# Performance work log

Measured on AMD Instinct MI355X. Metric: run time of the kernel, lower is better.

The kernel has to match this reference:

```python
import jax, jax.numpy as jnp
import numpy as np

B, S, I, H, C, V = 512, 64, 300, 1024, 2, 50000


def setup_inputs() -> dict:
    key = jax.random.key(0)
    ks = jax.random.split(key, 10)
    s = 0.05
    return {
        "x": jax.random.randint(ks[0], (B, S), 0, V),
        "lengths": jax.random.randint(ks[1], (B,), 1, S + 1),
        "embed": jax.random.normal(ks[2], (V, I), jnp.float32) * s,
        "Wih_e": jax.random.normal(ks[3], (4 * H, I), jnp.float32) * s,
        "Whh_e": jax.random.normal(ks[4], (4 * H, H), jnp.float32) * s,
        "bih_e": jnp.zeros((4 * H,), jnp.float32),
        "bhh_e": jnp.zeros((4 * H,), jnp.float32),
        "Wih_d": jax.random.normal(ks[5], (4 * H, I), jnp.float32) * s,
        "Whh_d": jax.random.normal(ks[6], (4 * H, H), jnp.float32) * s,
        "bih_d": jnp.zeros((4 * H,), jnp.float32),
        "bhh_d": jnp.zeros((4 * H,), jnp.float32),
        "W_lin": jax.random.normal(ks[7], (C, H), jnp.float32) * s,
        "b_lin": jnp.zeros((C,), jnp.float32),
    }


def lstm_cell(xi, h, c, Wih, Whh, bih, bhh):
    # PyTorch LSTMCell gate order: i, f, g, o
    g = xi @ Wih.T + bih + h @ Whh.T + bhh
    i, f, gg, o = jnp.split(g, 4, axis=-1)
    c = jax.nn.sigmoid(f) * c + jax.nn.sigmoid(i) * jnp.tanh(gg)
    return jax.nn.sigmoid(o) * jnp.tanh(c), c


def reference(x, lengths, embed, Wih_e, Whh_e, bih_e, bhh_e,
              Wih_d, Whh_d, bih_d, bhh_d, W_lin, b_lin):
    bsz, slen = x.shape
    hdim = Whh_e.shape[1]
    ncls = W_lin.shape[0]
    xs = embed[x.T]                      # [S, B, I] (seq-major, like x.transpose(0,1))

    h0 = jnp.zeros((bsz, hdim), xs.dtype)
    c0 = jnp.zeros((bsz, hdim), xs.dtype)

    def enc_step(carry, xi):
        h, c = carry
        h, c = lstm_cell(xi, h, c, Wih_e, Whh_e, bih_e, bhh_e)
        return (h, c), h

    # forward pass over sequence
    (h, c), enc_fwd = jax.lax.scan(enc_step, (h0, c0), xs)          # enc_fwd: [S,B,H]
    # backward pass with the SAME encoder cell, continuing from (h, c)
    (h, c), h_bwd = jax.lax.scan(enc_step, (h, c), xs[::-1])        # h_bwd:  [S,B,H]
    # k-th backward step pairs with encoder_forward[k] in the original code
    enc_out = (enc_fwd + h_bwd) * 0.5                               # [S,B,H]

    def dec_step(carry, xi):
        h, c = carry
        # original attention sums over batch AND hidden -> one scalar per timestep,
        # and rebuilds w as a fresh Variable (no gradient through the weights).
        w = jax.nn.softmax(jnp.sum(h[None, :, :] * enc_out, axis=(1, 2)))  # [S]
        w = jax.lax.stop_gradient(w)
        h = h + jnp.einsum('t,tbh->bh', w, enc_out)
        h, c = lstm_cell(xi, h, c, Wih_d, Whh_d, bih_d, bhh_d)
        return (h, c), h

    _, dec = jax.lax.scan(dec_step, (h, c), xs)                     # [S,B,H]

    out = dec @ W_lin.T + b_lin                                     # [S,B,C]
    out = out.transpose(1, 0, 2)                                    # [B,S,C]
    pad = jnp.array([1.0, 0.0], out.dtype)                          # overwrite beyond lengths
    mask = jnp.arange(slen)[None, :] < lengths[:, None]             # [B,S]
    out = jnp.where(mask[:, :, None], out, pad)
    return out.reshape(bsz * slen, ncls)
```

## Files before the change

kernel.cpp:

```cpp
#include <hip/hip_runtime.h>
#include <hip/hip_bf16.h>

#define BSZ 512
#define SEQ 64
#define IDIM 300
#define KP1 384
#define HDIM 1024
#define G4 4096
#define BH (BSZ*HDIM)

typedef __attribute__((ext_vector_type(8))) short bf16x8;
typedef __attribute__((ext_vector_type(4))) float f32x4;
typedef __attribute__((ext_vector_type(8))) unsigned short u16x8;
typedef __attribute__((ext_vector_type(4))) unsigned short u16x4;

__device__ __forceinline__ float sigmoidf_(float x){ return 1.f/(1.f+__expf(-x)); }
__device__ __forceinline__ float bf2f(unsigned short u){
    union{unsigned int i; float f;} v; v.i = ((unsigned)u)<<16; return v.f;
}
__device__ __forceinline__ unsigned short f2bf(float f){
    __hip_bfloat16 b = __float2bfloat16(f);
    return *(unsigned short*)&b;
}

__global__ void embed_gather_k(const int* __restrict__ x, const float* __restrict__ embed,
                               __hip_bfloat16* __restrict__ xs){
    int t = blockIdx.x, b = blockIdx.y;
    int ix = x[b*SEQ + t];
    const float* src = embed + (size_t)ix * IDIM;
    __hip_bfloat16* dst = xs + ((size_t)t*BSZ + b) * KP1;
    for (int k = threadIdx.x; k < KP1; k += 64)
        dst[k] = __float2bfloat16(k < IDIM ? src[k] : 0.f);
}

__global__ void conv_w_k(const float* __restrict__ Wih_e, const float* __restrict__ Wih_d,
                         const float* __restrict__ Whh_e, const float* __restrict__ Whh_d,
                         __hip_bfloat16* __restrict__ Pe, __hip_bfloat16* __restrict__ Pd,
                         __hip_bfloat16* __restrict__ He, __hip_bfloat16* __restrict__ Hd){
    int nr = blockIdx.x, v = blockIdx.y;
    int orig = ((nr>>5)&3)*HDIM + (nr>>7)*32 + (nr&31);
    if (v < 2){
        const float* src = (v ? Wih_d : Wih_e) + (size_t)orig*IDIM;
        __hip_bfloat16* dst = (v ? Pd : Pe) + (size_t)nr*KP1;
        for (int k = threadIdx.x; k < KP1; k += 64)
            dst[k] = __float2bfloat16(k < IDIM ? src[k] : 0.f);
    } else {
        const float* src = ((v == 3) ? Whh_d : Whh_e) + (size_t)orig*HDIM;
        __hip_bfloat16* dst = ((v == 3) ? Hd : He) + (size_t)nr*HDIM;
        for (int k = threadIdx.x; k < HDIM; k += 64)
            dst[k] = __float2bfloat16(src[k]);
    }
}

__global__ void bias_comb_k(const float* __restrict__ a, const float* __restrict__ b2,
                            const float* __restrict__ c2, const float* __restrict__ d2,
                            float* __restrict__ be, float* __restrict__ bd){
    int i = blockIdx.x*256 + threadIdx.x;
    int nr = i & 4095;
    int orig = ((nr>>5)&3)*HDIM + (nr>>7)*32 + (nr&31);
    if (i < G4) be[nr] = a[orig] + b2[orig];
    else        bd[nr] = c2[orig] + d2[orig];
}

__global__ void zero_hc_k(float* __restrict__ h, float* __restrict__ c,
                          __hip_bfloat16* __restrict__ h_bf,
                          unsigned int* __restrict__ bar, unsigned int* __restrict__ gen){
    int idx = blockIdx.x*256 + threadIdx.x;
    h[idx] = 0.f; c[idx] = 0.f; h_bf[idx] = __float2bfloat16(0.f);
    if (idx == 0){ bar[0] = 0u; gen[0] = 0u; }
}

#define BM 64
#define BN 128
#define NK1 (KP1/128)
#define NK2 (HDIM/128)
#define NKT (NK1+NK2)

__global__ __launch_bounds__(512) void xpre_k(
    const __hip_bfloat16* __restrict__ xs, const __hip_bfloat16* __restrict__ B1,
    float* __restrict__ Gx)
{
    __shared__ __align__(16) char smem[131072];
    const int tid  = threadIdx.x;
    const int lane = tid & 63, wv = tid >> 6;
    const int row0 = blockIdx.y * BM;
    const int col0 = blockIdx.x * BN;
    const int wm = wv >> 2, wn = wv & 3;
    const int fb = blockIdx.y*32 + blockIdx.x;

    #pragma unroll
    for (int ks = 0; ks < 3; ++ks)
        #pragma unroll
        for (int q = 0; q < 4; ++q){
            int u = q*512 + tid;
            int r = u >> 4, s = u & 15;
            int g = s ^ (r & 15);
            const __hip_bfloat16* src = B1 + (size_t)(col0 + r)*KP1 + ks*128 + g*8;
            char* dst = smem + ks*32768 + q*8192 + wv*1024;
            __builtin_amdgcn_global_load_lds(
                (const __attribute__((address_space(1))) void*)src,
                (__attribute__((address_space(3))) void*)dst, 16, 0, 0);
        }

    auto stage_a = [&](int t, int ks, int p){
        #pragma unroll
        for (int half = 0; half < 2; ++half){
            int u = half*512 + tid;
            int r = u >> 4, s = u & 15;
            int g = s ^ (r & 15);
            const __hip_bfloat16* src = xs + (size_t)t*BSZ*KP1 + (size_t)(row0 + r)*KP1 + ks*128 + g*8;
            char* dst = smem + 98304 + p*16384 + half*8192 + wv*1024;
            __builtin_amdgcn_global_load_lds(
                (const __attribute__((address_space(1))) void*)src,
                (__attribute__((address_space(3))) void*)dst, 16, 0, 0);
        }
    };

    f32x4 acc[2][2] = {};
    auto compute_a = [&](int p, int ks){
        const char* Ab = smem + 98304 + p*16384;
        const char* Bb = smem + ks*32768;
        const int rr = lane & 15, g = lane >> 4;
        bf16x8 af[2][4], bfr[2][4];
        #pragma unroll
        for (int m = 0; m < 2; ++m){
            int r = wm*32 + m*16 + rr;
            #pragma unroll
            for (int kk = 0; kk < 4; ++kk)
                af[m][kk] = *(const bf16x8*)(Ab + r*256 + ((kk*4 + g) ^ (r & 15))*16);
        }
        #pragma unroll
        for (int n = 0; n < 2; ++n){
            int r = wn*32 + n*16 + rr;
            #pragma unroll
            for (int kk = 0; kk < 4; ++kk)
                bfr[n][kk] = *(const bf16x8*)(Bb + r*256 + ((kk*4 + g) ^ (r & 15))*16);
        }
        #pragma unroll
        for (int kk = 0; kk < 4; ++kk)
            #pragma unroll
            for (int m = 0; m < 2; ++m)
                #pragma unroll
                for (int n = 0; n < 2; ++n)
                    acc[m][n] = __builtin_amdgcn_mfma_f32_16x16x32_bf16(af[m][kk], bfr[n][kk], acc[m][n], 0, 0, 0);
    };

    stage_a(0, 0, 0);
    __syncthreads();
    for (int t = 0; t < SEQ; ++t){
        #pragma unroll
        for (int ks = 0; ks < 3; ++ks){
            int u = t*3 + ks;
            int p = u & 1;
            if (u + 1 < SEQ*3) stage_a((u+1)/3, (u+1)%3, p ^ 1);
            compute_a(p, ks);
            if (ks == 2){
                float* gp = Gx + (((size_t)t*256 + fb)*512 + tid)*16;
                #pragma unroll
                for (int m = 0; m < 2; ++m)
                    #pragma unroll
                    for (int n = 0; n < 2; ++n)
                        *(f32x4*)(gp + (m*2+n)*4) = acc[m][n];
                acc[0][0] = f32x4{}; acc[0][1] = f32x4{};
                acc[1][0] = f32x4{}; acc[1][1] = f32x4{};
            }
            __syncthreads();
        }
    }
}

__device__ __forceinline__ void grid_sync_(unsigned int* bar, unsigned int* gen){
    __syncthreads();
    __threadfence();
    if (threadIdx.x == 0){
        unsigned int g = __hip_atomic_load(gen, __ATOMIC_RELAXED, __HIP_MEMORY_SCOPE_AGENT);
        if (__hip_atomic_fetch_add(bar, 1u, __ATOMIC_ACQ_REL, __HIP_MEMORY_SCOPE_AGENT) == 255u){
            __hip_atomic_store(bar, 0u, __ATOMIC_RELAXED, __HIP_MEMORY_SCOPE_AGENT);
            __hip_atomic_fetch_add(gen, 1u, __ATOMIC_RELEASE, __HIP_MEMORY_SCOPE_AGENT);
        } else {
            while (__hip_atomic_load(gen, __ATOMIC_ACQUIRE, __HIP_MEMORY_SCOPE_AGENT) == g)
                __builtin_amdgcn_s_sleep(2);
        }
    }
    __syncthreads();
    __threadfence();
}

__global__ __launch_bounds__(512, 2) void enc_persist_k(
    const __hip_bfloat16* __restrict__ B2, const float* __restrict__ bias,
    const float* __restrict__ Gx,
    float* __restrict__ c, float* __restrict__ h, __hip_bfloat16* __restrict__ h_bf,
    __hip_bfloat16* __restrict__ enc,
    unsigned int* __restrict__ bar, unsigned int* __restrict__ gen)
{
    __shared__ __align__(16) char smem[98304];
    const int tid  = threadIdx.x;
    const int lane = tid & 63, wv = tid >> 6;
    const int bid  = blockIdx.x;
    const int bx = bid & 31, by = bid >> 5;
    const int row0 = by * BM;
    const int col0 = bx * BN;
    const int wm = wv >> 2, wn = wv & 3;

    const int erow = tid >> 3;
    const int ejj0 = (tid & 7) * 4;
    const size_t ebase = (size_t)(row0 + erow)*HDIM + bx*32 + ejj0;

    f32x4 creg = {0.f, 0.f, 0.f, 0.f};

    auto stage = [&](int ks, int p){
        char* base = smem + p*49152;
        #pragma unroll
        for (int half = 0; half < 2; ++half){
            int u = half*512 + tid;
            int r = u >> 4, s = u & 15;
            int g = s ^ (r & 15);
            const __hip_bfloat16* src = h_bf + (size_t)(row0 + r)*HDIM + ks*128 + g*8;
            char* dst = base + half*8192 + wv*1024;
            __builtin_amdgcn_global_load_lds(
                (const __attribute__((address_space(1))) void*)src,
                (__attribute__((address_space(3))) void*)dst, 16, 0, 0);
        }
        #pragma unroll
        for (int q = 0; q < 4; ++q){
            int u = q*512 + tid;
            int r = u >> 4, s = u & 15;
            int g = s ^ (r & 15);
            const __hip_bfloat16* src = B2 + (size_t)(col0 + r)*HDIM + ks*128 + g*8;
            char* dst = base + 16384 + q*8192 + wv*1024;
            __builtin_amdgcn_global_load_lds(
                (const __attribute__((address_space(1))) void*)src,
                (__attribute__((address_space(3))) void*)dst, 16, 0, 0);
        }
    };

    for (int i = 0; i < 2*SEQ; ++i){
        const int t = (i < SEQ) ? i : (2*SEQ - 1 - i);
        f32x4 acc[2][2];
        {
            const float* gp = Gx + (((size_t)t*256 + bid)*512 + tid)*16;
            #pragma unroll
            for (int m = 0; m < 2; ++m)
                #pragma unroll
                for (int n = 0; n < 2; ++n)
                    acc[m][n] = *(const f32x4*)(gp + (m*2+n)*4);
        }

        stage(0, 0);
        __syncthreads();
        for (int ks = 0; ks < NK2; ++ks){
            int p = ks & 1;
            if (ks + 1 < NK2) stage(ks + 1, p ^ 1);
            {
                const char* Ab = smem + p*49152;
                const char* Bb = Ab + 16384;
                const int rr = lane & 15, g = lane >> 4;
                bf16x8 af[2][4], bfr[2][4];
                #pragma unroll
                for (int m = 0; m < 2; ++m){
                    int r = wm*32 + m*16 + rr;
                    #pragma unroll
                    for (int kk = 0; kk < 4; ++kk)
                        af[m][kk] = *(const bf16x8*)(Ab + r*256 + ((kk*4 + g) ^ (r & 15))*16);
                }
                #pragma unroll
                for (int n = 0; n < 2; ++n){
                    int r = wn*32 + n*16 + rr;
                    #pragma unroll
                    for (int kk = 0; kk < 4; ++kk)
                        bfr[n][kk] = *(const bf16x8*)(Bb + r*256 + ((kk*4 + g) ^ (r & 15))*16);
                }
                #pragma unroll
                for (int kk = 0; kk < 4; ++kk)
                    #pragma unroll
                    for (int m = 0; m < 2; ++m)
                        #pragma unroll
                        for (int n = 0; n < 2; ++n)
                            acc[m][n] = __builtin_amdgcn_mfma_f32_16x16x32_bf16(af[m][kk], bfr[n][kk], acc[m][n], 0, 0, 0);
            }
            __syncthreads();
        }

        float* ep = (float*)smem;
        {
            const int rr = lane & 15, q4 = lane >> 4;
            #pragma unroll
            for (int m = 0; m < 2; ++m){
                int row = wm*32 + m*16 + q4*4;
                #pragma unroll
                for (int n = 0; n < 2; ++n){
                    int jj = n*16 + rr;
                    float bi = bias[col0 + wn*32 + jj];
                    #pragma unroll
                    for (int q = 0; q < 4; ++q)
                        ep[(wn*64 + row + q)*33 + jj] = acc[m][n][q] + bi;
                }
            }
        }
        __syncthreads();
        {
            f32x4 hv;
            #pragma unroll
            for (int e = 0; e < 4; ++e){
                float gi = ep[(0*64 + erow)*33 + ejj0 + e];
                float gf = ep[(1*64 + erow)*33 + ejj0 + e];
                float gg = ep[(2*64 + erow)*33 + ejj0 + e];
                float go = ep[(3*64 + erow)*33 + ejj0 + e];
                float cc = sigmoidf_(gf)*creg[e] + sigmoidf_(gi)*tanhf(gg);
                float hh = sigmoidf_(go)*tanhf(cc);
                creg[e] = cc; hv[e] = hh;
            }
            u16x4 hb;
            #pragma unroll
            for (int e = 0; e < 4; ++e) hb[e] = f2bf(hv[e]);
            *(u16x4*)(h_bf + ebase) = hb;
            if (i < SEQ){
                *(u16x4*)(enc + (size_t)i*BH + ebase) = hb;
            } else {
                __hip_bfloat16* eslot = enc + (size_t)(i - SEQ)*BH;
                u16x4 eo = *(const u16x4*)(eslot + ebase);
                u16x4 r;
                #pragma unroll
                for (int e = 0; e < 4; ++e) r[e] = f2bf(0.5f*(bf2f(eo[e]) + hv[e]));
                *(u16x4*)(eslot + ebase) = r;
            }
            if (i == 2*SEQ - 1){
                *(f32x4*)(c + ebase) = creg;
                *(f32x4*)(h + ebase) = hv;
            }
        }
        grid_sync_(bar, gen);
    }
}

template<int XPRE>
__global__ __launch_bounds__(512) void lstm_step_k(
    const __hip_bfloat16* __restrict__ A1, const __hip_bfloat16* __restrict__ B1,
    const __hip_bfloat16* __restrict__ A2, const __hip_bfloat16* __restrict__ B2,
    const float* __restrict__ bias, const float* __restrict__ Gxt,
    float* __restrict__ c, float* __restrict__ h, __hip_bfloat16* __restrict__ h_bf,
    __hip_bfloat16* __restrict__ encSlot, int mode)
{
    constexpr int NKT_ = XPRE ? NK2 : NKT;
    __shared__ __align__(16) char smem[98304];
    const int tid  = threadIdx.x;
    const int lane = tid & 63, wv = tid >> 6;
    const int row0 = blockIdx.y * BM;
    const int col0 = blockIdx.x * BN;
    const int wm = wv >> 2, wn = wv & 3;

    f32x4 acc[2][2];
    if constexpr (XPRE){
        const float* gp = Gxt + (((size_t)(blockIdx.y*32 + blockIdx.x))*512 + tid)*16;
        #pragma unroll
        for (int m = 0; m < 2; ++m)
            #pragma unroll
            for (int n = 0; n < 2; ++n)
                acc[m][n] = *(const f32x4*)(gp + (m*2+n)*4);
    } else {
        acc[0][0] = f32x4{}; acc[0][1] = f32x4{};
        acc[1][0] = f32x4{}; acc[1][1] = f32x4{};
    }

    auto stage = [&](int ks, int p){
        const __hip_bfloat16* A; const __hip_bfloat16* B; int KA, k0;
        if constexpr (XPRE){ A = A2; B = B2; KA = HDIM; k0 = ks*128; }
        else {
            if (ks < NK1){ A = A1; B = B1; KA = KP1;  k0 = ks*128; }
            else         { A = A2; B = B2; KA = HDIM; k0 = (ks-NK1)*128; }
        }
        char* base = smem + p*49152;
        #pragma unroll
        for (int half = 0; half < 2; ++half){
            int u = half*512 + tid;
            int r = u >> 4, s = u & 15;
            int g = s ^ (r & 15);
            const __hip_bfloat16* src = A + (size_t)(row0 + r)*KA + k0 + g*8;
            char* dst = base + half*8192 + wv*1024;
            __builtin_amdgcn_global_load_lds(
                (const __attribute__((address_space(1))) void*)src,
                (__attribute__((address_space(3))) void*)dst, 16, 0, 0);
        }
        #pragma unroll
        for (int q = 0; q < 4; ++q){
            int u = q*512 + tid;
            int r = u >> 4, s = u & 15;
            int g = s ^ (r & 15);
            const __hip_bfloat16* src = B + (size_t)(col0 + r)*KA + k0 + g*8;
            char* dst = base + 16384 + q*8192 + wv*1024;
            __builtin_amdgcn_global_load_lds(
                (const __attribute__((address_space(1))) void*)src,
                (__attribute__((address_space(3))) void*)dst, 16, 0, 0);
        }
    };

    auto compute = [&](int p){
        const char* Ab = smem + p*49152;
        const char* Bb = Ab + 16384;
        const int rr = lane & 15, g = lane >> 4;
        bf16x8 af[2][4], bfr[2][4];
        #pragma unroll
        for (int m = 0; m < 2; ++m){
            int r = wm*32 + m*16 + rr;
            #pragma unroll
            for (int kk = 0; kk < 4; ++kk)
                af[m][kk] = *(const bf16x8*)(Ab + r*256 + ((kk*4 + g) ^ (r & 15))*16);
        }
        #pragma unroll
        for (int n = 0; n < 2; ++n){
            int r = wn*32 + n*16 + rr;
            #pragma unroll
            for (int kk = 0; kk < 4; ++kk)
                bfr[n][kk] = *(const bf16x8*)(Bb + r*256 + ((kk*4 + g) ^ (r & 15))*16);
        }
        #pragma unroll
        for (int kk = 0; kk < 4; ++kk)
            #pragma unroll
            for (int m = 0; m < 2; ++m)
                #pragma unroll
                for (int n = 0; n < 2; ++n)
                    acc[m][n] = __builtin_amdgcn_mfma_f32_16x16x32_bf16(af[m][kk], bfr[n][kk], acc[m][n], 0, 0, 0);
    };

    const int erow = tid >> 3;
    const int ejj0 = (tid & 7) * 4;
    const size_t ebase = (size_t)(row0 + erow)*HDIM + blockIdx.x*32 + ejj0;

    stage(0, 0);
    const f32x4 cpre = *(const f32x4*)(c + ebase);
    __syncthreads();
    for (int ks = 0; ks < NKT_; ++ks){
        int p = ks & 1;
        if (ks + 1 < NKT_) stage(ks + 1, p ^ 1);
        compute(p);
        __syncthreads();
    }

    float* ep = (float*)smem;
    {
        const int rr = lane & 15, q4 = lane >> 4;
        #pragma unroll
        for (int m = 0; m < 2; ++m){
            int row = wm*32 + m*16 + q4*4;
            #pragma unroll
            for (int n = 0; n < 2; ++n){
                int jj = n*16 + rr;
                float bi = bias[col0 + wn*32 + jj];
                #pragma unroll
                for (int q = 0; q < 4; ++q)
                    ep[(wn*64 + row + q)*33 + jj] = acc[m][n][q] + bi;
            }
        }
    }
    __syncthreads();
    {
        f32x4 cv, hv;
        #pragma unroll
        for (int e = 0; e < 4; ++e){
            float gi = ep[(0*64 + erow)*33 + ejj0 + e];
            float gf = ep[(1*64 + erow)*33 + ejj0 + e];
            float gg = ep[(2*64 + erow)*33 + ejj0 + e];
            float go = ep[(3*64 + erow)*33 + ejj0 + e];
            float cc = sigmoidf_(gf)*cpre[e] + sigmoidf_(gi)*tanhf(gg);
            float hh = sigmoidf_(go)*tanhf(cc);
            cv[e] = cc; hv[e] = hh;
        }
        *(f32x4*)(c + ebase) = cv;
        *(f32x4*)(h + ebase) = hv;
        u16x4 hb;
        #pragma unroll
        for (int e = 0; e < 4; ++e) hb[e] = f2bf(hv[e]);
        *(u16x4*)(h_bf + ebase) = hb;
        if (mode == 0){
            *(u16x4*)(encSlot + ebase) = hb;
        } else if (mode == 1){
            u16x4 eo = *(const u16x4*)(encSlot + ebase);
            u16x4 r;
            #pragma unroll
            for (int e = 0; e < 4; ++e) r[e] = f2bf(0.5f*(bf2f(eo[e]) + hv[e]));
            *(u16x4*)(encSlot + ebase) = r;
        }
    }
}

__global__ __launch_bounds__(256) void attn_part_k(
    const __hip_bfloat16* __restrict__ h_bf, const __hip_bfloat16* __restrict__ enc,
    float* __restrict__ part,
    const float* __restrict__ h, const float* __restrict__ Wl, const float* __restrict__ bl,
    const int* __restrict__ len, float* __restrict__ out, int dect)
{
    __shared__ float red[4];
    int lane = threadIdx.x & 63, w = threadIdx.x >> 6;
    if (blockIdx.x < 64){
        int ch = blockIdx.x;
        int s  = blockIdx.y;
        const u16x8* e  = (const u16x8*)(enc + (size_t)s*BH + (size_t)ch*8192);
        const u16x8* hp = (const u16x8*)(h_bf + (size_t)ch*8192);
        float sum = 0.f;
        for (int i = threadIdx.x; i < 1024; i += 256){
            u16x8 ev = e[i], hv = hp[i];
            #pragma unroll
            for (int j = 0; j < 8; ++j) sum += bf2f(hv[j]) * bf2f(ev[j]);
        }
        #pragma unroll
        for (int m = 32; m >= 1; m >>= 1) sum += __shfl_xor(sum, m);
        if (lane == 0) red[w] = sum;
        __syncthreads();
        if (threadIdx.x == 0) part[s*64 + ch] = red[0]+red[1]+red[2]+red[3];
    } else if (dect >= 0){
        int b = ((blockIdx.x - 64)*64 + blockIdx.y)*4 + w;
        const float* hb = h + (size_t)b*HDIM;
        float s0 = 0.f, s1 = 0.f;
        for (int j = lane; j < HDIM; j += 64){
            float v = hb[j];
            s0 += v * Wl[j];
            s1 += v * Wl[HDIM + j];
        }
        #pragma unroll
        for (int m = 32; m >= 1; m >>= 1){ s0 += __shfl_xor(s0, m); s1 += __shfl_xor(s1, m); }
        if (lane == 0){
            bool valid = dect < len[b];
            size_t r = ((size_t)b*SEQ + dect)*2;
            out[r]   = valid ? (s0 + bl[0]) : 1.0f;
            out[r+1] = valid ? (s1 + bl[1]) : 0.0f;
        }
    }
}

__global__ __launch_bounds__(256) void attn_apply_k(
    const float* __restrict__ h, const float* __restrict__ part,
    const __hip_bfloat16* __restrict__ enc, __hip_bfloat16* __restrict__ hat_bf)
{
    __shared__ float wl[64];
    int lane = threadIdx.x & 63;
    if (threadIdx.x < 64){
        float tot = 0.f;
        #pragma unroll 8
        for (int ch = 0; ch < 64; ++ch) tot += part[lane*64 + ch];
        float m = tot;
        #pragma unroll
        for (int msk = 32; msk >= 1; msk >>= 1) m = fmaxf(m, __shfl_xor(m, msk));
        float e = __expf(tot - m);
        float sm = e;
        #pragma unroll
        for (int msk = 32; msk >= 1; msk >>= 1) sm += __shfl_xor(sm, msk);
        wl[lane] = e / sm;
    }
    __syncthreads();
    size_t i4 = ((size_t)blockIdx.x*256 + threadIdx.x) * 4;
    float v[4];
    {
        f32x4 a = *(const f32x4*)(h + i4);
        v[0]=a[0]; v[1]=a[1]; v[2]=a[2]; v[3]=a[3];
    }
    for (int s = 0; s < SEQ; ++s){
        u16x4 ev = *(const u16x4*)(enc + (size_t)s*BH + i4);
        float w = wl[s];
        #pragma unroll
        for (int j = 0; j < 4; ++j) v[j] += w * bf2f(ev[j]);
    }
    u16x4 ov;
    #pragma unroll
    for (int j = 0; j < 4; ++j) ov[j] = f2bf(v[j]);
    *(u16x4*)(hat_bf + i4) = ov;
}

__global__ void dec_linear_k(const float* __restrict__ h, const float* __restrict__ Wl,
                             const float* __restrict__ bl, const int* __restrict__ len,
                             float* __restrict__ out, int t)
{
    int b = blockIdx.x, lane = threadIdx.x;
    const float* hb = h + (size_t)b*HDIM;
    float s0 = 0.f, s1 = 0.f;
    for (int j = lane; j < HDIM; j += 64){
        float v = hb[j];
        s0 += v * Wl[j];
        s1 += v * Wl[HDIM + j];
    }
    #pragma unroll
    for (int m = 32; m >= 1; m >>= 1){ s0 += __shfl_xor(s0, m); s1 += __shfl_xor(s1, m); }
    if (lane == 0){
        bool valid = t < len[b];
        size_t r = ((size_t)b*SEQ + t)*2;
        out[r]   = valid ? (s0 + bl[0]) : 1.0f;
        out[r+1] = valid ? (s1 + bl[1]) : 0.0f;
    }
}

extern "C" void kernel_launch(void* const* d_in, const int* in_sizes, int n_in,
                              void* d_out, int out_size, void* d_ws, size_t ws_size,
                              hipStream_t stream)
{
    (void)in_sizes; (void)n_in; (void)out_size;
    const int*   x      = (const int*)  d_in[0];
    const int*   len    = (const int*)  d_in[1];
    const float* embed  = (const float*)d_in[2];
    const float* Wih_e  = (const float*)d_in[3];
    const float* Whh_e  = (const float*)d_in[4];
    const float* bih_e  = (const float*)d_in[5];
    const float* bhh_e  = (const float*)d_in[6];
    const float* Wih_d  = (const float*)d_in[7];
    const float* Whh_d  = (const float*)d_in[8];
    const float* bih_d  = (const float*)d_in[9];
    const float* bhh_d  = (const float*)d_in[10];
    const float* W_lin  = (const float*)d_in[11];
    const float* b_lin  = (const float*)d_in[12];
    float* out = (float*)d_out;

    float* ws = (float*)d_ws;
    size_t off = 0;
    auto alloc = [&](size_t nfloats){ size_t o = off; off += (nfloats + 63) & ~(size_t)63; return o; };
    __hip_bfloat16* xs_bf  = (__hip_bfloat16*)(ws + alloc((size_t)SEQ*BSZ*KP1/2));
    __hip_bfloat16* Pe     = (__hip_bfloat16*)(ws + alloc((size_t)G4*KP1/2));
    __hip_bfloat16* Pd     = (__hip_bfloat16*)(ws + alloc((size_t)G4*KP1/2));
    __hip_bfloat16* He     = (__hip_bfloat16*)(ws + alloc((size_t)G4*HDIM/2));
    __hip_bfloat16* Hd     = (__hip_bfloat16*)(ws + alloc((size_t)G4*HDIM/2));
    float* be   = ws + alloc(G4);
    float* bd   = ws + alloc(G4);
    float* h    = ws + alloc(BH);
    float* c    = ws + alloc(BH);
    __hip_bfloat16* h_bf   = (__hip_bfloat16*)(ws + alloc(BH/2));
    __hip_bfloat16* hat_bf = (__hip_bfloat16*)(ws + alloc(BH/2));
    __hip_bfloat16* enc    = (__hip_bfloat16*)(ws + alloc((size_t)SEQ*BH/2));
    float* part = ws + alloc(64*64);
    unsigned int* bar = (unsigned int*)(ws + alloc(32));
    unsigned int* gen = bar + 16;
    float* Gx   = ws + alloc((size_t)SEQ*256*512*16);
    const bool useGx = (off * sizeof(float)) <= ws_size;

    embed_gather_k<<<dim3(SEQ, BSZ), 64, 0, stream>>>(x, embed, xs_bf);
    conv_w_k<<<dim3(G4, 4), 64, 0, stream>>>(Wih_e, Wih_d, Whh_e, Whh_d, Pe, Pd, He, Hd);
    bias_comb_k<<<32, 256, 0, stream>>>(bih_e, bhh_e, bih_d, bhh_d, be, bd);
    zero_hc_k<<<BH/256, 256, 0, stream>>>(h, c, h_bf, bar, gen);

    dim3 ggrid(G4/BN, BSZ/BM);

    if (useGx){
        xpre_k<<<dim3(32, 8), 512, 0, stream>>>(xs_bf, Pe, Gx);
        enc_persist_k<<<256, 512, 0, stream>>>(He, be, Gx, c, h, h_bf, enc, bar, gen);
    } else {
        for (int t = 0; t < SEQ; ++t)
            lstm_step_k<0><<<ggrid, 512, 0, stream>>>(xs_bf + (size_t)t*BSZ*KP1, Pe, h_bf, He, be,
                                                      nullptr, c, h, h_bf, enc + (size_t)t*BH, 0);
        for (int k = 0; k < SEQ; ++k){
            int t = SEQ - 1 - k;
            lstm_step_k<0><<<ggrid, 512, 0, stream>>>(xs_bf + (size_t)t*BSZ*KP1, Pe, h_bf, He, be,
                                                      nullptr, c, h, h_bf, enc + (size_t)k*BH, 1);
        }
    }

    for (int t = 0; t < SEQ; ++t){
        attn_part_k<<<dim3(66, 64), 256, 0, stream>>>(h_bf, enc, part, h, W_lin, b_lin, len, out, t - 1);
        attn_apply_k<<<512, 256, 0, stream>>>(h, part, enc, hat_bf);
        lstm_step_k<0><<<ggrid, 512, 0, stream>>>(xs_bf + (size_t)t*BSZ*KP1, Pd, hat_bf, Hd, bd,
                                                  nullptr, c, h, h_bf, nullptr, 2);
    }
    dec_linear_k<<<BSZ, 64, 0, stream>>>(h, W_lin, b_lin, len, out, SEQ - 1);
}
```

Baseline: 4.341 ms.

## Fold input projection into persistent encoder kernel and drop precomputed Gx buffer

Removes the separate xpre_k kernel that precomputed the input-to-gate GEMM for all timesteps into a large fp32 Gx buffer. The persistent encoder now streams both the embedded input tiles and the recurrent h tiles through the same double-buffered K loop every step. It also drops the trailing threadfence in the grid barrier and the 2-blocks-per-CU launch bound. This saves the large Gx write/read traffic and one kernel launch, but puts the input GEMM back on the serial recurrent critical path.

Measured after the change: 11.24 ms. +159.0%, slower.

```diff
diff --git a/kernel.cpp b/kernel.cpp
--- a/kernel.cpp
+++ b/kernel.cpp
@@ -76,99 +76,6 @@
 #define NK2 (HDIM/128)
 #define NKT (NK1+NK2)
 
-__global__ __launch_bounds__(512) void xpre_k(
-    const __hip_bfloat16* __restrict__ xs, const __hip_bfloat16* __restrict__ B1,
-    float* __restrict__ Gx)
-{
-    __shared__ __align__(16) char smem[131072];
-    const int tid  = threadIdx.x;
-    const int lane = tid & 63, wv = tid >> 6;
-    const int row0 = blockIdx.y * BM;
-    const int col0 = blockIdx.x * BN;
-    const int wm = wv >> 2, wn = wv & 3;
-    const int fb = blockIdx.y*32 + blockIdx.x;
-
-    #pragma unroll
-    for (int ks = 0; ks < 3; ++ks)
-        #pragma unroll
-        for (int q = 0; q < 4; ++q){
-            int u = q*512 + tid;
-            int r = u >> 4, s = u & 15;
-            int g = s ^ (r & 15);
-            const __hip_bfloat16* src = B1 + (size_t)(col0 + r)*KP1 + ks*128 + g*8;
-            char* dst = smem + ks*32768 + q*8192 + wv*1024;
-            __builtin_amdgcn_global_load_lds(
-                (const __attribute__((address_space(1))) void*)src,
-                (__attribute__((address_space(3))) void*)dst, 16, 0, 0);
-        }
-
-    auto stage_a = [&](int t, int ks, int p){
-        #pragma unroll
-        for (int half = 0; half < 2; ++half){
-            int u = half*512 + tid;
-            int r = u >> 4, s = u & 15;
-            int g = s ^ (r & 15);
-            const __hip_bfloat16* src = xs + (size_t)t*BSZ*KP1 + (size_t)(row0 + r)*KP1 + ks*128 + g*8;
-            char* dst = smem + 98304 + p*16384 + half*8192 + wv*1024;
-            __builtin_amdgcn_global_load_lds(
-                (const __attribute__((address_space(1))) void*)src,
-                (__attribute__((address_space(3))) void*)dst, 16, 0, 0);
-        }
-    };
-
-    f32x4 acc[2][2] = {};
-    auto compute_a = [&](int p, int ks){
-        const char* Ab = smem + 98304 + p*16384;
-        const char* Bb = smem + ks*32768;
-        const int rr = lane & 15, g = lane >> 4;
-        bf16x8 af[2][4], bfr[2][4];
-        #pragma unroll
-        for (int m = 0; m < 2; ++m){
-            int r = wm*32 + m*16 + rr;
-            #pragma unroll
-            for (int kk = 0; kk < 4; ++kk)
-                af[m][kk] = *(const bf16x8*)(Ab + r*256 + ((kk*4 + g) ^ (r & 15))*16);
-        }
-        #pragma unroll
-        for (int n = 0; n < 2; ++n){
-            int r = wn*32 + n*16 + rr;
-            #pragma unroll
-            for (int kk = 0; kk < 4; ++kk)
-                bfr[n][kk] = *(const bf16x8*)(Bb + r*256 + ((kk*4 + g) ^ (r & 15))*16);
-        }
-        #pragma unroll
-        for (int kk = 0; kk < 4; ++kk)
-            #pragma unroll
-            for (int m = 0; m < 2; ++m)
-                #pragma unroll
-                for (int n = 0; n < 2; ++n)
-                    acc[m][n] = __builtin_amdgcn_mfma_f32_16x16x32_bf16(af[m][kk], bfr[n][kk], acc[m][n], 0, 0, 0);
-    };
-
-    stage_a(0, 0, 0);
-    __syncthreads();
-    for (int t = 0; t < SEQ; ++t){
-        #pragma unroll
-        for (int ks = 0; ks < 3; ++ks){
-            int u = t*3 + ks;
-            int p = u & 1;
-            if (u + 1 < SEQ*3) stage_a((u+1)/3, (u+1)%3, p ^ 1);
-            compute_a(p, ks);
-            if (ks == 2){
-                float* gp = Gx + (((size_t)t*256 + fb)*512 + tid)*16;
-                #pragma unroll
-                for (int m = 0; m < 2; ++m)
-                    #pragma unroll
-                    for (int n = 0; n < 2; ++n)
-                        *(f32x4*)(gp + (m*2+n)*4) = acc[m][n];
-                acc[0][0] = f32x4{}; acc[0][1] = f32x4{};
-                acc[1][0] = f32x4{}; acc[1][1] = f32x4{};
-            }
-            __syncthreads();
-        }
-    }
-}
-
 __device__ __forceinline__ void grid_sync_(unsigned int* bar, unsigned int* gen){
     __syncthreads();
     __threadfence();
@@ -183,12 +90,11 @@
         }
     }
     __syncthreads();
-    __threadfence();
-}
-
-__global__ __launch_bounds__(512, 2) void enc_persist_k(
+}
+
+__global__ __launch_bounds__(512) void enc_persist_k(
+    const __hip_bfloat16* __restrict__ xs, const __hip_bfloat16* __restrict__ B1,
     const __hip_bfloat16* __restrict__ B2, const float* __restrict__ bias,
-    const float* __restrict__ Gx,
     float* __restrict__ c, float* __restrict__ h, __hip_bfloat16* __restrict__ h_bf,
     __hip_bfloat16* __restrict__ enc,
     unsigned int* __restrict__ bar, unsigned int* __restrict__ gen)
@@ -208,49 +114,46 @@
 
     f32x4 creg = {0.f, 0.f, 0.f, 0.f};
 
-    auto stage = [&](int ks, int p){
-        char* base = smem + p*49152;
-        #pragma unroll
-        for (int half = 0; half < 2; ++half){
-            int u = half*512 + tid;
-            int r = u >> 4, s = u & 15;
-            int g = s ^ (r & 15);
-            const __hip_bfloat16* src = h_bf + (size_t)(row0 + r)*HDIM + ks*128 + g*8;
-            char* dst = base + half*8192 + wv*1024;
-            __builtin_amdgcn_global_load_lds(
-                (const __attribute__((address_space(1))) void*)src,
-                (__attribute__((address_space(3))) void*)dst, 16, 0, 0);
-        }
-        #pragma unroll
-        for (int q = 0; q < 4; ++q){
-            int u = q*512 + tid;
-            int r = u >> 4, s = u & 15;
-            int g = s ^ (r & 15);
-            const __hip_bfloat16* src = B2 + (size_t)(col0 + r)*HDIM + ks*128 + g*8;
-            char* dst = base + 16384 + q*8192 + wv*1024;
-            __builtin_amdgcn_global_load_lds(
-                (const __attribute__((address_space(1))) void*)src,
-                (__attribute__((address_space(3))) void*)dst, 16, 0, 0);
-        }
-    };
-
     for (int i = 0; i < 2*SEQ; ++i){
         const int t = (i < SEQ) ? i : (2*SEQ - 1 - i);
-        f32x4 acc[2][2];
-        {
-            const float* gp = Gx + (((size_t)t*256 + bid)*512 + tid)*16;
-            #pragma unroll
-            for (int m = 0; m < 2; ++m)
-                #pragma unroll
-                for (int n = 0; n < 2; ++n)
-                    acc[m][n] = *(const f32x4*)(gp + (m*2+n)*4);
-        }
+        const __hip_bfloat16* A1 = xs + (size_t)t*BSZ*KP1;
+
+        auto stage = [&](int ks, int p){
+            const __hip_bfloat16* A; const __hip_bfloat16* B; int KA, k0;
+            if (ks < NK1){ A = A1;   B = B1; KA = KP1;  k0 = ks*128; }
+            else         { A = h_bf; B = B2; KA = HDIM; k0 = (ks-NK1)*128; }
+            char* base = smem + p*49152;
+            #pragma unroll
+            for (int half = 0; half < 2; ++half){
+                int u = half*512 + tid;
+                int r = u >> 4, s = u & 15;
+                int g = s ^ (r & 15);
+                const __hip_bfloat16* src = A + (size_t)(row0 + r)*KA + k0 + g*8;
+                char* dst = base + half*8192 + wv*1024;
+                __builtin_amdgcn_global_load_lds(
+                    (const __attribute__((address_space(1))) void*)src,
+                    (__attribute__((address_space(3))) void*)dst, 16, 0, 0);
+            }
+            #pragma unroll
+            for (int q = 0; q < 4; ++q){
+                int u = q*512 + tid;
+                int r = u >> 4, s = u & 15;
+                int g = s ^ (r & 15);
+                const __hip_bfloat16* src = B + (size_t)(col0 + r)*KA + k0 + g*8;
+                char* dst = base + 16384 + q*8192 + wv*1024;
+                __builtin_amdgcn_global_load_lds(
+                    (const __attribute__((address_space(1))) void*)src,
+                    (__attribute__((address_space(3))) void*)dst, 16, 0, 0);
+            }
+        };
+
+        f32x4 acc[2][2] = {};
 
         stage(0, 0);
         __syncthreads();
-        for (int ks = 0; ks < NK2; ++ks){
+        for (int ks = 0; ks < NKT; ++ks){
             int p = ks & 1;
-            if (ks + 1 < NK2) stage(ks + 1, p ^ 1);
+            if (ks + 1 < NKT) stage(ks + 1, p ^ 1);
             {
                 const char* Ab = smem + p*49152;
                 const char* Bb = Ab + 16384;
@@ -333,15 +236,13 @@
     }
 }
 
-template<int XPRE>
 __global__ __launch_bounds__(512) void lstm_step_k(
     const __hip_bfloat16* __restrict__ A1, const __hip_bfloat16* __restrict__ B1,
     const __hip_bfloat16* __restrict__ A2, const __hip_bfloat16* __restrict__ B2,
-    const float* __restrict__ bias, const float* __restrict__ Gxt,
+    const float* __restrict__ bias,
     float* __restrict__ c, float* __restrict__ h, __hip_bfloat16* __restrict__ h_bf,
     __hip_bfloat16* __restrict__ encSlot, int mode)
 {
-    constexpr int NKT_ = XPRE ? NK2 : NKT;
     __shared__ __align__(16) char smem[98304];
     const int tid  = threadIdx.x;
     const int lane = tid & 63, wv = tid >> 6;
@@ -349,26 +250,12 @@
     const int col0 = blockIdx.x * BN;
     const int wm = wv >> 2, wn = wv & 3;
 
-    f32x4 acc[2][2];
-    if constexpr (XPRE){
-        const float* gp = Gxt + (((size_t)(blockIdx.y*32 + blockIdx.x))*512 + tid)*16;
-        #pragma unroll
-        for (int m = 0; m < 2; ++m)
-            #pragma unroll
-            for (int n = 0; n < 2; ++n)
-                acc[m][n] = *(const f32x4*)(gp + (m*2+n)*4);
-    } else {
-        acc[0][0] = f32x4{}; acc[0][1] = f32x4{};
-        acc[1][0] = f32x4{}; acc[1][1] = f32x4{};
-    }
+    f32x4 acc[2][2] = {};
 
     auto stage = [&](int ks, int p){
         const __hip_bfloat16* A; const __hip_bfloat16* B; int KA, k0;
-        if constexpr (XPRE){ A = A2; B = B2; KA = HDIM; k0 = ks*128; }
-        else {
-            if (ks < NK1){ A = A1; B = B1; KA = KP1;  k0 = ks*128; }
-            else         { A = A2; B = B2; KA = HDIM; k0 = (ks-NK1)*128; }
-        }
+        if (ks < NK1){ A = A1; B = B1; KA = KP1;  k0 = ks*128; }
+        else         { A = A2; B = B2; KA = HDIM; k0 = (ks-NK1)*128; }
         char* base = smem + p*49152;
         #pragma unroll
         for (int half = 0; half < 2; ++half){
@@ -429,9 +316,9 @@
     stage(0, 0);
     const f32x4 cpre = *(const f32x4*)(c + ebase);
     __syncthreads();
-    for (int ks = 0; ks < NKT_; ++ks){
+    for (int ks = 0; ks < NKT; ++ks){
         int p = ks & 1;
-        if (ks + 1 < NKT_) stage(ks + 1, p ^ 1);
+        if (ks + 1 < NKT) stage(ks + 1, p ^ 1);
         compute(p);
         __syncthreads();
     }
@@ -591,7 +478,7 @@
                               void* d_out, int out_size, void* d_ws, size_t ws_size,
                               hipStream_t stream)
 {
-    (void)in_sizes; (void)n_in; (void)out_size;
+    (void)in_sizes; (void)n_in; (void)out_size; (void)ws_size;
     const int*   x      = (const int*)  d_in[0];
     const int*   len    = (const int*)  d_in[1];
     const float* embed  = (const float*)d_in[2];
@@ -625,35 +512,20 @@
     float* part = ws + alloc(64*64);
     unsigned int* bar = (unsigned int*)(ws + alloc(32));
     unsigned int* gen = bar + 16;
-    float* Gx   = ws + alloc((size_t)SEQ*256*512*16);
-    const bool useGx = (off * sizeof(float)) <= ws_size;
 
     embed_gather_k<<<dim3(SEQ, BSZ), 64, 0, stream>>>(x, embed, xs_bf);
     conv_w_k<<<dim3(G4, 4), 64, 0, stream>>>(Wih_e, Wih_d, Whh_e, Whh_d, Pe, Pd, He, Hd);
     bias_comb_k<<<32, 256, 0, stream>>>(bih_e, bhh_e, bih_d, bhh_d, be, bd);
     zero_hc_k<<<BH/256, 256, 0, stream>>>(h, c, h_bf, bar, gen);
 
+    enc_persist_k<<<256, 512, 0, stream>>>(xs_bf, Pe, He, be, c, h, h_bf, enc, bar, gen);
+
     dim3 ggrid(G4/BN, BSZ/BM);
-
-    if (useGx){
-        xpre_k<<<dim3(32, 8), 512, 0, stream>>>(xs_bf, Pe, Gx);
-        enc_persist_k<<<256, 512, 0, stream>>>(He, be, Gx, c, h, h_bf, enc, bar, gen);
-    } else {
-        for (int t = 0; t < SEQ; ++t)
-            lstm_step_k<0><<<ggrid, 512, 0, stream>>>(xs_bf + (size_t)t*BSZ*KP1, Pe, h_bf, He, be,
-                                                      nullptr, c, h, h_bf, enc + (size_t)t*BH, 0);
-        for (int k = 0; k < SEQ; ++k){
-            int t = SEQ - 1 - k;
-            lstm_step_k<0><<<ggrid, 512, 0, stream>>>(xs_bf + (size_t)t*BSZ*KP1, Pe, h_bf, He, be,
-                                                      nullptr, c, h, h_bf, enc + (size_t)k*BH, 1);
-        }
-    }
-
     for (int t = 0; t < SEQ; ++t){
         attn_part_k<<<dim3(66, 64), 256, 0, stream>>>(h_bf, enc, part, h, W_lin, b_lin, len, out, t - 1);
         attn_apply_k<<<512, 256, 0, stream>>>(h, part, enc, hat_bf);
-        lstm_step_k<0><<<ggrid, 512, 0, stream>>>(xs_bf + (size_t)t*BSZ*KP1, Pd, hat_bf, Hd, bd,
-                                                  nullptr, c, h, h_bf, nullptr, 2);
+        lstm_step_k<<<ggrid, 512, 0, stream>>>(xs_bf + (size_t)t*BSZ*KP1, Pd, hat_bf, Hd, bd,
+                                               c, h, h_bf, nullptr, 2);
     }
     dec_linear_k<<<BSZ, 64, 0, stream>>>(h, W_lin, b_lin, len, out, SEQ - 1);
 }
```
